# Performance work log

Measured on AMD Instinct MI355X. Metric: run time of the kernel, lower is better.

## Reference

```python
import jax, jax.numpy as jnp
import numpy as np

NQ, N, C = 8192, 32768, 128


def setup_inputs() -> dict:
    key = jax.random.key(0)
    k1, k2, k3 = jax.random.split(key, 3)
    return {
        "query_pos": jax.random.normal(k1, (NQ, 3), dtype=jnp.float32),
        "neural_feat": jax.random.normal(k2, (N, C), dtype=jnp.float32),
        "neural_pos": jax.random.normal(k3, (N, 3), dtype=jnp.float32),
        "knn": 64,
    }


def _cdist(a, b):
    # Euclidean pairwise distances via the (|a|^2 + |b|^2 - 2ab) expansion.
    a2 = jnp.sum(a * a, axis=-1, keepdims=True)          # [N',1]
    b2 = jnp.sum(b * b, axis=-1)                          # [N]
    d2 = a2 + b2[None, :] - 2.0 * (a @ b.T)               # [N',N]
    return jnp.sqrt(jnp.maximum(d2, 1e-12))


def reference(query_pos, neural_feat, neural_pos, knn):
    dists = _cdist(query_pos, neural_pos)                 # [N',N]
    # torch.topk(largest=False, sorted=True) == top_k of negated dists.
    neg_vals, closest_ind = jax.lax.top_k(-dists, knn)    # [N',k]
    closest_dists = -neg_vals                             # ascending
    closest_feat = neural_feat[closest_ind]               # [N',k,C] gather
    inv_dist = 1.0 / (closest_dists + 1e-5)               # [N',k]
    retrieved_feat = jnp.sum(closest_feat * inv_dist[..., None], axis=1)  # [N',C]
    return retrieved_feat
```

## Files before the change

### kernel.cpp

```cpp
#include <hip/hip_runtime.h>
#include <math.h>

#define NQ    8192
#define NPTS  32768
#define KNN   64
#define QPB   4
#define CAPW  56
#define NBLK  (NQ / QPB)
#define PPW   (NPTS / 4)
#define NGRP  (PPW / 256)
#define MAXM  224

__device__ __forceinline__ unsigned key_of(float f) {
  unsigned u = __float_as_uint(f);
  return (u & 0x80000000u) ? ~u : (u | 0x80000000u);
}
__device__ __forceinline__ float val_of(unsigned k) {
  unsigned u = (k & 0x80000000u) ? (k & 0x7fffffffu) : ~k;
  return __uint_as_float(u);
}
__device__ __forceinline__ int mbcnt64(unsigned long long m) {
  return __builtin_amdgcn_mbcnt_hi((unsigned)(m >> 32),
         __builtin_amdgcn_mbcnt_lo((unsigned)m, 0));
}
__device__ __forceinline__ float rflf(float x) {
  return __int_as_float(__builtin_amdgcn_readfirstlane(__float_as_int(x)));
}
__device__ __forceinline__ int rfli(int x) { return __builtin_amdgcn_readfirstlane(x); }

__device__ __forceinline__ float norm_cdf(float x) { return 0.5f * erfcf(-x * 0.70710678f); }
__device__ __forceinline__ float ball_mass(float mu, float r) {
  float a = r - mu, b = r + mu;
  float e = __expf(-0.5f * b * b) - __expf(-0.5f * a * a);
  return e / (mu * 2.50662827f) + norm_cdf(a) - norm_cdf(-mu) + norm_cdf(b) - norm_cdf(mu);
}

__global__ __launch_bounds__(256, 8) void ft_knn_kernel(
    const float* __restrict__ qpos, const float* __restrict__ feat,
    const float* __restrict__ pos, float* __restrict__ out) {

  __shared__ uint2 sCand[QPB][4][CAPW];
  __shared__ uint2 sSel[QPB][KNN];
  __shared__ int   sCntW[4][QPB];
  __shared__ float sQ[QPB][4];
  __shared__ float sTau[QPB], sTlo[QPB], sThi[QPB];
  __shared__ int   sAct[QPB], sAny;

  const int tid   = threadIdx.x;
  const int lane  = tid & 63;
  const int wv    = tid >> 6;
  const int qbase = blockIdx.x * QPB;

  if (tid < QPB) {
    int gq = qbase + tid;
    float x = qpos[gq * 3 + 0], y = qpos[gq * 3 + 1], z = qpos[gq * 3 + 2];
    float b = x * x + y * y + z * z;
    sQ[tid][0] = -2.f * x; sQ[tid][1] = -2.f * y; sQ[tid][2] = -2.f * z; sQ[tid][3] = b;
    float mu = fmaxf(sqrtf(b), 0.05f);
    const float target = 110.0f / 32768.0f;
    float lo = 0.f, hi = mu + 8.f;
    for (int i = 0; i < 16; ++i) {
      float r = 0.5f * (lo + hi);
      if (ball_mass(mu, r) < target) lo = r; else hi = r;
    }
    sTau[tid] = hi * hi;
    sTlo[tid] = 0.f; sThi[tid] = -1.f;
    sAct[tid] = 1;
  }
  __syncthreads();

  for (int attempt = 0; attempt < 12; ++attempt) {
    float qx[QPB], qy[QPB], qz[QPB], bq[QPB], tq[QPB]; int act[QPB], cnt[QPB];
    #pragma unroll
    for (int q = 0; q < QPB; ++q) {
      qx[q] = rflf(sQ[q][0]); qy[q] = rflf(sQ[q][1]); qz[q] = rflf(sQ[q][2]);
      bq[q] = rflf(sQ[q][3]);
      act[q] = rfli(sAct[q]);
      float tau = rflf(sTau[q]);
      tq[q] = act[q] ? (tau - bq[q]) : -1e30f;
      cnt[q] = 0;
    }
    if (act[0] | act[1] | act[2] | act[3]) {
      const int pw = wv * PPW;
      for (int g = 0; g < NGRP; ++g) {
        const int pt = pw + g * 256 + lane * 4;
        const float* bp = pos + (size_t)pt * 3;
        const float4 A  = *(const float4*)(bp);
        const float4 B  = *(const float4*)(bp + 4);
        const float4 Cc = *(const float4*)(bp + 8);
        const float x0 = A.x,  y0 = A.y,  z0 = A.z;
        const float x1 = A.w,  y1 = B.x,  z1 = B.y;
        const float x2 = B.z,  y2 = B.w,  z2 = Cc.x;
        const float x3 = Cc.y, y3 = Cc.z, z3 = Cc.w;
        const float n0 = x0 * x0 + y0 * y0 + z0 * z0;
        const float n1 = x1 * x1 + y1 * y1 + z1 * z1;
        const float n2 = x2 * x2 + y2 * y2 + z2 * z2;
        const float n3 = x3 * x3 + y3 * y3 + z3 * z3;
        #pragma unroll
        for (int q = 0; q < QPB; ++q) {
          float d0 = fmaf(z0, qz[q], fmaf(y0, qy[q], fmaf(x0, qx[q], n0)));
          float d1 = fmaf(z1, qz[q], fmaf(y1, qy[q], fmaf(x1, qx[q], n1)));
          float d2 = fmaf(z2, qz[q], fmaf(y2, qy[q], fmaf(x2, qx[q], n2)));
          float d3 = fmaf(z3, qz[q], fmaf(y3, qy[q], fmaf(x3, qx[q], n3)));
          const bool h0 = d0 < tq[q], h1 = d1 < tq[q], h2 = d2 < tq[q], h3 = d3 < tq[q];
          const unsigned long long m0 = __ballot(h0), m1 = __ballot(h1),
                                   m2 = __ballot(h2), m3 = __ballot(h3);
          if (m0) { int p = cnt[q] + mbcnt64(m0);
                    if (h0 && p < CAPW) sCand[q][wv][p] = make_uint2(key_of(d0 + bq[q]), (unsigned)(pt + 0));
                    cnt[q] += (int)__popcll(m0); }
          if (m1) { int p = cnt[q] + mbcnt64(m1);
                    if (h1 && p < CAPW) sCand[q][wv][p] = make_uint2(key_of(d1 + bq[q]), (unsigned)(pt + 1));
                    cnt[q] += (int)__popcll(m1); }
          if (m2) { int p = cnt[q] + mbcnt64(m2);
                    if (h2 && p < CAPW) sCand[q][wv][p] = make_uint2(key_of(d2 + bq[q]), (unsigned)(pt + 2));
                    cnt[q] += (int)__popcll(m2); }
          if (m3) { int p = cnt[q] + mbcnt64(m3);
                    if (h3 && p < CAPW) sCand[q][wv][p] = make_uint2(key_of(d3 + bq[q]), (unsigned)(pt + 3));
                    cnt[q] += (int)__popcll(m3); }
        }
      }
    }
    __syncthreads();
    if (lane == 0) {
      #pragma unroll
      for (int q = 0; q < QPB; ++q) if (act[q]) sCntW[wv][q] = cnt[q];
    }
    if (tid == 0) sAny = 0;
    __syncthreads();
    if (tid < QPB && sAct[tid]) {
      int tot = 0, ovf = 0;
      #pragma unroll
      for (int w = 0; w < 4; ++w) { int c = sCntW[w][tid]; ovf |= (c > CAPW); tot += c; }
      if (!ovf && tot >= KNN && tot <= MAXM) sAct[tid] = 0;
      else {
        if (!ovf && tot < KNN) { sTlo[tid] = sTau[tid];
          sTau[tid] = (sThi[tid] < 0.f) ? sTau[tid] * 3.f : 0.5f * (sTau[tid] + sThi[tid]); }
        else { sThi[tid] = sTau[tid]; sTau[tid] = 0.5f * (sTlo[tid] + sTau[tid]); }
        sAny = 1;
      }
    }
    __syncthreads();
    if (!sAny) break;
  }

  {
    const int q = wv;
    const int c0 = rfli(min(sCntW[0][q], CAPW));
    const int c1 = rfli(min(sCntW[1][q], CAPW));
    const int c2 = rfli(min(sCntW[2][q], CAPW));
    const int c3 = rfli(min(sCntW[3][q], CAPW));
    const int P1 = c0, P2 = P1 + c1, P3 = P2 + c2, m = P3 + c3;

    unsigned k[4], id[4];
    #pragma unroll
    for (int s = 0; s < 4; ++s) {
      const int g = s * 64 + lane;
      const int ge1 = g >= P1, ge2 = g >= P2, ge3 = g >= P3;
      const int w = ge1 + ge2 + ge3;
      const int sb = ge3 ? P3 : (ge2 ? P2 : (ge1 ? P1 : 0));
      uint2 kv = make_uint2(0xFFFFFFFFu, 0u);
      if (g < m) kv = sCand[q][w][g - sb];
      k[s] = kv.x; id[s] = kv.y;
    }

    unsigned lo = 0u, hi = 0xFFFFFFFFu;
    for (int it = 0; it < 32; ++it) {
      unsigned mid = lo + ((hi - lo) >> 1);
      int c = (int)(__popcll(__ballot(k[0] <= mid)) + __popcll(__ballot(k[1] <= mid)) +
                    __popcll(__ballot(k[2] <= mid)) + __popcll(__ballot(k[3] <= mid)));
      if (c >= KNN) hi = mid; else lo = mid + 1;
    }
    const unsigned K = lo;

    int fill = 0;
    #pragma unroll
    for (int s = 0; s < 4; ++s) {
      const bool lt = k[s] < K;
      const unsigned long long msk = __ballot(lt);
      if (msk) {
        const int p = fill + mbcnt64(msk);
        if (lt) { float dv = val_of(k[s]);
                  float w_ = 1.f / (sqrtf(fmaxf(dv, 1e-12f)) + 1e-5f);
                  sSel[q][p] = make_uint2(id[s], __float_as_uint(w_)); }
        fill += (int)__popcll(msk);
      }
    }
    #pragma unroll
    for (int s = 0; s < 4; ++s) {
      const bool eq = (k[s] == K);
      const unsigned long long msk = __ballot(eq);
      if (msk) {
        const int p = fill + mbcnt64(msk);
        if (eq && p < KNN) { float dv = val_of(k[s]);
                             float w_ = 1.f / (sqrtf(fmaxf(dv, 1e-12f)) + 1e-5f);
                             sSel[q][p] = make_uint2(id[s], __float_as_uint(w_)); }
        fill += (int)__popcll(msk);
      }
    }
  }

  {
    const int q = wv, gq = qbase + wv;
    float ax = 0.f, ay = 0.f;
    #pragma unroll 8
    for (int j = 0; j < KNN; ++j) {
      const uint2 pr = sSel[q][j];
      const float w = __uint_as_float(pr.y);
      const float2 f2 = *(const float2*)(feat + ((size_t)pr.x << 7) + (lane << 1));
      ax = fmaf(w, f2.x, ax);
      ay = fmaf(w, f2.y, ay);
    }
    *(float2*)(out + ((size_t)gq << 7) + (lane << 1)) = make_float2(ax, ay);
  }
}

extern "C" void kernel_launch(void* const* d_in, const int* in_sizes, int n_in,
                              void* d_out, int out_size, void* d_ws, size_t ws_size,
                              hipStream_t stream) {
  const float* qpos = (const float*)d_in[0];
  const float* feat = (const float*)d_in[1];
  const float* pos  = (const float*)d_in[2];
  float* out = (float*)d_out;
  ft_knn_kernel<<<dim3(NBLK), dim3(256), 0, stream>>>(qpos, feat, pos, out);
}
```

Before: 143.8 us.

## Replace brute-force radius scan with uniform grid binning of points

Builds a 32^3 uniform grid over the neural points each call (zero, histogram, prefix scan, scatter kernels), then each wave handles one query and scans only the cells overlapping its current search radius, retrying with an adjusted radius as before. This avoids every query block streaming all 32768 points per attempt. It adds four small launches, atomics, and a single-block prefix scan. Each wave now adjusts its radius independently, without block-wide syncs. The grid bounds are fixed at ±4.8, so points outside are clamped into edge cells.

```diff
diff --git a/kernel.cpp b/kernel.cpp
--- a/kernel.cpp
+++ b/kernel.cpp
@@ -4,12 +4,11 @@
 #define NQ    8192
 #define NPTS  32768
 #define KNN   64
-#define QPB   4
-#define CAPW  56
-#define NBLK  (NQ / QPB)
-#define PPW   (NPTS / 4)
-#define NGRP  (PPW / 256)
-#define MAXM  224
+#define CAP   256
+#define G     32
+#define NCELLS (G*G*G)
+#define GLO   (-4.8f)
+#define GINV  (G / 9.6f)
 
 __device__ __forceinline__ unsigned key_of(float f) {
   unsigned u = __float_as_uint(f);
@@ -35,142 +34,145 @@
   return e / (mu * 2.50662827f) + norm_cdf(a) - norm_cdf(-mu) + norm_cdf(b) - norm_cdf(mu);
 }
 
-__global__ __launch_bounds__(256, 8) void ft_knn_kernel(
-    const float* __restrict__ qpos, const float* __restrict__ feat,
-    const float* __restrict__ pos, float* __restrict__ out) {
-
-  __shared__ uint2 sCand[QPB][4][CAPW];
-  __shared__ uint2 sSel[QPB][KNN];
-  __shared__ int   sCntW[4][QPB];
-  __shared__ float sQ[QPB][4];
-  __shared__ float sTau[QPB], sTlo[QPB], sThi[QPB];
-  __shared__ int   sAct[QPB], sAny;
-
-  const int tid   = threadIdx.x;
-  const int lane  = tid & 63;
-  const int wv    = tid >> 6;
-  const int qbase = blockIdx.x * QPB;
-
-  if (tid < QPB) {
-    int gq = qbase + tid;
-    float x = qpos[gq * 3 + 0], y = qpos[gq * 3 + 1], z = qpos[gq * 3 + 2];
-    float b = x * x + y * y + z * z;
-    sQ[tid][0] = -2.f * x; sQ[tid][1] = -2.f * y; sQ[tid][2] = -2.f * z; sQ[tid][3] = b;
-    float mu = fmaxf(sqrtf(b), 0.05f);
+__device__ __forceinline__ int cidx(float v) {
+  int i = (int)floorf((v - GLO) * GINV);
+  return min(max(i, 0), G - 1);
+}
+
+
+__global__ __launch_bounds__(1024) void zero_kernel(int* __restrict__ cnt) {
+  cnt[blockIdx.x * 1024 + threadIdx.x] = 0;
+}
+
+__global__ __launch_bounds__(256) void hist_tau_kernel(
+    const float* __restrict__ pos, const float* __restrict__ qpos,
+    int* __restrict__ cnt, float* __restrict__ tau) {
+  const int gid = blockIdx.x * 256 + threadIdx.x;
+  const float x = pos[gid * 3 + 0], y = pos[gid * 3 + 1], z = pos[gid * 3 + 2];
+  const int c = (cidx(z) * G + cidx(y)) * G + cidx(x);
+  atomicAdd(&cnt[c], 1);
+  if (gid < NQ) {
+    const float qx = qpos[gid * 3 + 0], qy = qpos[gid * 3 + 1], qz = qpos[gid * 3 + 2];
+    const float b = qx * qx + qy * qy + qz * qz;
+    const float mu = fmaxf(sqrtf(b), 0.05f);
     const float target = 110.0f / 32768.0f;
     float lo = 0.f, hi = mu + 8.f;
     for (int i = 0; i < 16; ++i) {
       float r = 0.5f * (lo + hi);
       if (ball_mass(mu, r) < target) lo = r; else hi = r;
     }
-    sTau[tid] = hi * hi;
-    sTlo[tid] = 0.f; sThi[tid] = -1.f;
-    sAct[tid] = 1;
-  }
+    tau[gid] = hi * hi;
+  }
+}
+
+__global__ __launch_bounds__(1024) void prefix_kernel(
+    int* __restrict__ cnt, int* __restrict__ start) {
+  __shared__ int sSum[1024];
+  const int t = threadIdx.x;
+  const int base = t * 32;
+  int local[32];
+  int s = 0;
+  #pragma unroll
+  for (int j = 0; j < 32; ++j) { local[j] = s; s += cnt[base + j]; }
+  sSum[t] = s;
   __syncthreads();
+  for (int off = 1; off < 1024; off <<= 1) {
+    int v = (t >= off) ? sSum[t - off] : 0;
+    __syncthreads();
+    sSum[t] += v;
+    __syncthreads();
+  }
+  const int excl = (t == 0) ? 0 : sSum[t - 1];
+  #pragma unroll
+  for (int j = 0; j < 32; ++j) {
+    const int v = excl + local[j];
+    start[base + j] = v;
+    cnt[base + j] = v;
+  }
+  if (t == 1023) start[NCELLS] = excl + s;
+}
+
+__global__ __launch_bounds__(256) void scatter_kernel(
+    const float* __restrict__ pos, int* __restrict__ cursor, float4* __restrict__ pts) {
+  const int gid = blockIdx.x * 256 + threadIdx.x;
+  const float x = pos[gid * 3 + 0], y = pos[gid * 3 + 1], z = pos[gid * 3 + 2];
+  const int c = (cidx(z) * G + cidx(y)) * G + cidx(x);
+  const int slot = atomicAdd(&cursor[c], 1);
+  pts[slot] = make_float4(x, y, z, __int_as_float(gid));
+}
+
+
+__global__ __launch_bounds__(256, 8) void knn_main(
+    const float* __restrict__ qpos, const float* __restrict__ feat,
+    const int* __restrict__ cellStart, const float4* __restrict__ pts,
+    const float* __restrict__ tauArr, float* __restrict__ out) {
+
+  __shared__ uint2 sCand[4][CAP];
+  __shared__ uint2 sSel[4][KNN];
+
+  const int tid = threadIdx.x, lane = tid & 63, wv = tid >> 6;
+  const int gq = blockIdx.x * 4 + wv;
+
+  const float qx = rflf(qpos[gq * 3 + 0]);
+  const float qy = rflf(qpos[gq * 3 + 1]);
+  const float qz = rflf(qpos[gq * 3 + 2]);
+  const float bq = qx * qx + qy * qy + qz * qz;
+  const float nx = -2.f * qx, ny = -2.f * qy, nz = -2.f * qz;
+  float r2 = rflf(tauArr[gq]);
+  float tlo = 0.f, thi = -1.f;
+  int cnt = 0;
 
   for (int attempt = 0; attempt < 12; ++attempt) {
-    float qx[QPB], qy[QPB], qz[QPB], bq[QPB], tq[QPB]; int act[QPB], cnt[QPB];
-    #pragma unroll
-    for (int q = 0; q < QPB; ++q) {
-      qx[q] = rflf(sQ[q][0]); qy[q] = rflf(sQ[q][1]); qz[q] = rflf(sQ[q][2]);
-      bq[q] = rflf(sQ[q][3]);
-      act[q] = rfli(sAct[q]);
-      float tau = rflf(sTau[q]);
-      tq[q] = act[q] ? (tau - bq[q]) : -1e30f;
-      cnt[q] = 0;
-    }
-    if (act[0] | act[1] | act[2] | act[3]) {
-      const int pw = wv * PPW;
-      for (int g = 0; g < NGRP; ++g) {
-        const int pt = pw + g * 256 + lane * 4;
-        const float* bp = pos + (size_t)pt * 3;
-        const float4 A  = *(const float4*)(bp);
-        const float4 B  = *(const float4*)(bp + 4);
-        const float4 Cc = *(const float4*)(bp + 8);
-        const float x0 = A.x,  y0 = A.y,  z0 = A.z;
-        const float x1 = A.w,  y1 = B.x,  z1 = B.y;
-        const float x2 = B.z,  y2 = B.w,  z2 = Cc.x;
-        const float x3 = Cc.y, y3 = Cc.z, z3 = Cc.w;
-        const float n0 = x0 * x0 + y0 * y0 + z0 * z0;
-        const float n1 = x1 * x1 + y1 * y1 + z1 * z1;
-        const float n2 = x2 * x2 + y2 * y2 + z2 * z2;
-        const float n3 = x3 * x3 + y3 * y3 + z3 * z3;
-        #pragma unroll
-        for (int q = 0; q < QPB; ++q) {
-          float d0 = fmaf(z0, qz[q], fmaf(y0, qy[q], fmaf(x0, qx[q], n0)));
-          float d1 = fmaf(z1, qz[q], fmaf(y1, qy[q], fmaf(x1, qx[q], n1)));
-          float d2 = fmaf(z2, qz[q], fmaf(y2, qy[q], fmaf(x2, qx[q], n2)));
-          float d3 = fmaf(z3, qz[q], fmaf(y3, qy[q], fmaf(x3, qx[q], n3)));
-          const bool h0 = d0 < tq[q], h1 = d1 < tq[q], h2 = d2 < tq[q], h3 = d3 < tq[q];
-          const unsigned long long m0 = __ballot(h0), m1 = __ballot(h1),
-                                   m2 = __ballot(h2), m3 = __ballot(h3);
-          if (m0) { int p = cnt[q] + mbcnt64(m0);
-                    if (h0 && p < CAPW) sCand[q][wv][p] = make_uint2(key_of(d0 + bq[q]), (unsigned)(pt + 0));
-                    cnt[q] += (int)__popcll(m0); }
-          if (m1) { int p = cnt[q] + mbcnt64(m1);
-                    if (h1 && p < CAPW) sCand[q][wv][p] = make_uint2(key_of(d1 + bq[q]), (unsigned)(pt + 1));
-                    cnt[q] += (int)__popcll(m1); }
-          if (m2) { int p = cnt[q] + mbcnt64(m2);
-                    if (h2 && p < CAPW) sCand[q][wv][p] = make_uint2(key_of(d2 + bq[q]), (unsigned)(pt + 2));
-                    cnt[q] += (int)__popcll(m2); }
-          if (m3) { int p = cnt[q] + mbcnt64(m3);
-                    if (h3 && p < CAPW) sCand[q][wv][p] = make_uint2(key_of(d3 + bq[q]), (unsigned)(pt + 3));
-                    cnt[q] += (int)__popcll(m3); }
+    const float r = sqrtf(r2);
+    const float tq = r2 - bq;
+    const int ix0 = cidx(qx - r), ix1 = cidx(qx + r);
+    const int iy0 = cidx(qy - r), iy1 = cidx(qy + r);
+    const int iz0 = cidx(qz - r), iz1 = cidx(qz + r);
+    cnt = 0;
+    for (int iz = iz0; iz <= iz1; ++iz) {
+      for (int iy = iy0; iy <= iy1; ++iy) {
+        const int rb = (iz * G + iy) * G;
+        const int s = rfli(cellStart[rb + ix0]);
+        const int e = rfli(cellStart[rb + ix1 + 1]);
+        for (int b = s; b < e; b += 64) {
+          const int o = b + lane;
+          const float4 P = pts[o];
+          const float n = P.x * P.x + P.y * P.y + P.z * P.z;
+          const float d = fmaf(P.z, nz, fmaf(P.y, ny, fmaf(P.x, nx, n)));
+          const bool h = (o < e) && (d < tq);
+          const unsigned long long m = __ballot(h);
+          if (m) {
+            const int p = cnt + mbcnt64(m);
+            if (h && p < CAP)
+              sCand[wv][p] = make_uint2(key_of(d + bq), __float_as_uint(P.w));
+            cnt += (int)__popcll(m);
+          }
         }
       }
     }
-    __syncthreads();
-    if (lane == 0) {
-      #pragma unroll
-      for (int q = 0; q < QPB; ++q) if (act[q]) sCntW[wv][q] = cnt[q];
-    }
-    if (tid == 0) sAny = 0;
-    __syncthreads();
-    if (tid < QPB && sAct[tid]) {
-      int tot = 0, ovf = 0;
-      #pragma unroll
-      for (int w = 0; w < 4; ++w) { int c = sCntW[w][tid]; ovf |= (c > CAPW); tot += c; }
-      if (!ovf && tot >= KNN && tot <= MAXM) sAct[tid] = 0;
-      else {
-        if (!ovf && tot < KNN) { sTlo[tid] = sTau[tid];
-          sTau[tid] = (sThi[tid] < 0.f) ? sTau[tid] * 3.f : 0.5f * (sTau[tid] + sThi[tid]); }
-        else { sThi[tid] = sTau[tid]; sTau[tid] = 0.5f * (sTlo[tid] + sTau[tid]); }
-        sAny = 1;
-      }
-    }
-    __syncthreads();
-    if (!sAny) break;
+    if (cnt >= KNN && cnt <= CAP) break;
+    if (cnt < KNN) { tlo = r2; r2 = (thi < 0.f) ? r2 * 3.f : 0.5f * (r2 + thi); }
+    else           { thi = r2; r2 = 0.5f * (tlo + r2); }
   }
 
   {
-    const int q = wv;
-    const int c0 = rfli(min(sCntW[0][q], CAPW));
-    const int c1 = rfli(min(sCntW[1][q], CAPW));
-    const int c2 = rfli(min(sCntW[2][q], CAPW));
-    const int c3 = rfli(min(sCntW[3][q], CAPW));
-    const int P1 = c0, P2 = P1 + c1, P3 = P2 + c2, m = P3 + c3;
-
+    const int mm = min(cnt, CAP);
     unsigned k[4], id[4];
     #pragma unroll
     for (int s = 0; s < 4; ++s) {
-      const int g = s * 64 + lane;
-      const int ge1 = g >= P1, ge2 = g >= P2, ge3 = g >= P3;
-      const int w = ge1 + ge2 + ge3;
-      const int sb = ge3 ? P3 : (ge2 ? P2 : (ge1 ? P1 : 0));
+      const int g2 = s * 64 + lane;
       uint2 kv = make_uint2(0xFFFFFFFFu, 0u);
-      if (g < m) kv = sCand[q][w][g - sb];
+      if (g2 < mm) kv = sCand[wv][g2];
       k[s] = kv.x; id[s] = kv.y;
     }
-
-    unsigned lo = 0u, hi = 0xFFFFFFFFu;
+    unsigned blo = 0u, bhi = 0xFFFFFFFFu;
     for (int it = 0; it < 32; ++it) {
-      unsigned mid = lo + ((hi - lo) >> 1);
-      int c = (int)(__popcll(__ballot(k[0] <= mid)) + __popcll(__ballot(k[1] <= mid)) +
-                    __popcll(__ballot(k[2] <= mid)) + __popcll(__ballot(k[3] <= mid)));
-      if (c >= KNN) hi = mid; else lo = mid + 1;
-    }
-    const unsigned K = lo;
+      const unsigned mid = blo + ((bhi - blo) >> 1);
+      const int c = (int)(__popcll(__ballot(k[0] <= mid)) + __popcll(__ballot(k[1] <= mid)) +
+                          __popcll(__ballot(k[2] <= mid)) + __popcll(__ballot(k[3] <= mid)));
+      if (c >= KNN) bhi = mid; else blo = mid + 1;
+    }
+    const unsigned K = blo;
 
     int fill = 0;
     #pragma unroll
@@ -179,9 +181,9 @@
       const unsigned long long msk = __ballot(lt);
       if (msk) {
         const int p = fill + mbcnt64(msk);
-        if (lt) { float dv = val_of(k[s]);
-                  float w_ = 1.f / (sqrtf(fmaxf(dv, 1e-12f)) + 1e-5f);
-                  sSel[q][p] = make_uint2(id[s], __float_as_uint(w_)); }
+        if (lt) { const float dv = val_of(k[s]);
+                  const float w_ = 1.f / (sqrtf(fmaxf(dv, 1e-12f)) + 1e-5f);
+                  sSel[wv][p] = make_uint2(id[s], __float_as_uint(w_)); }
         fill += (int)__popcll(msk);
       }
     }
@@ -191,20 +193,19 @@
       const unsigned long long msk = __ballot(eq);
       if (msk) {
         const int p = fill + mbcnt64(msk);
-        if (eq && p < KNN) { float dv = val_of(k[s]);
-                             float w_ = 1.f / (sqrtf(fmaxf(dv, 1e-12f)) + 1e-5f);
-                             sSel[q][p] = make_uint2(id[s], __float_as_uint(w_)); }
+        if (eq && p < KNN) { const float dv = val_of(k[s]);
+                             const float w_ = 1.f / (sqrtf(fmaxf(dv, 1e-12f)) + 1e-5f);
+                             sSel[wv][p] = make_uint2(id[s], __float_as_uint(w_)); }
         fill += (int)__popcll(msk);
       }
     }
   }
 
   {
-    const int q = wv, gq = qbase + wv;
     float ax = 0.f, ay = 0.f;
     #pragma unroll 8
     for (int j = 0; j < KNN; ++j) {
-      const uint2 pr = sSel[q][j];
+      const uint2 pr = sSel[wv][j];
       const float w = __uint_as_float(pr.y);
       const float2 f2 = *(const float2*)(feat + ((size_t)pr.x << 7) + (lane << 1));
       ax = fmaf(w, f2.x, ax);
@@ -221,5 +222,16 @@
   const float* feat = (const float*)d_in[1];
   const float* pos  = (const float*)d_in[2];
   float* out = (float*)d_out;
-  ft_knn_kernel<<<dim3(NBLK), dim3(256), 0, stream>>>(qpos, feat, pos, out);
-}
+
+  char* ws = (char*)d_ws;
+  int*    cnt   = (int*)(ws);
+  int*    start = (int*)(ws + (128 << 10));
+  float4* pts   = (float4*)(ws + (256 << 10) + 16);
+  float*  tau   = (float*)(ws + (256 << 10) + 16 + (size_t)(NPTS + 64) * 16);
+
+  zero_kernel   <<<dim3(NCELLS / 1024), dim3(1024), 0, stream>>>(cnt);
+  hist_tau_kernel<<<dim3(NPTS / 256),   dim3(256),  0, stream>>>(pos, qpos, cnt, tau);
+  prefix_kernel <<<dim3(1),             dim3(1024), 0, stream>>>(cnt, start);
+  scatter_kernel<<<dim3(NPTS / 256),    dim3(256),  0, stream>>>(pos, cnt, pts);
+  knn_main      <<<dim3(NQ / 4),        dim3(256),  0, stream>>>(qpos, feat, start, pts, tau, out);
+}
```

New measurement: 192.1 us. 1.34x slower.
